# Kernel optimization log

Measured on AMD Instinct MI355X. Metric: run time of the kernel, lower is better.

## Reference

```python
import jax, jax.numpy as jnp
import numpy as np

B, N, DOP, DM, H = 8, 2048, 256, 256, 256  # batch, n_ops==n_machines, dims


def setup_inputs() -> dict:
    key = jax.random.key(0)
    ks = jax.random.split(key, 21)
    s = 0.02
    inp = {
        "operation_features": jax.random.normal(ks[0], (B, N, DOP), jnp.float32),
        "machine_features": jax.random.normal(ks[1], (B, N, DM), jnp.float32),
        "type_match_mask": jax.random.bernoulli(ks[2], 0.3, (B, N, N)).astype(jnp.float32),
        "same_type_mask": jax.random.bernoulli(ks[3], 0.3, (B, N, N)).astype(jnp.float32),
        "oma_q_w": jax.random.normal(ks[4], (H, DM), jnp.float32) * s,
        "oma_q_b": jnp.zeros((H,), jnp.float32),
        "oma_kv_w": jax.random.normal(ks[5], (2 * H, DOP), jnp.float32) * s,
        "oma_kv_b": jnp.zeros((2 * H,), jnp.float32),
        "oma_s_w": jax.random.normal(ks[6], (1, 2 * H), jnp.float32) * s,
        "oma_s_b": jnp.zeros((1,), jnp.float32),
        "oma_o_w": jax.random.normal(ks[7], (DM, H), jnp.float32) * s,
        "oma_o_b": jnp.zeros((DM,), jnp.float32),
        "sa_w_w": jax.random.normal(ks[8], (3 * H, DM), jnp.float32) * s,
        "sa_w_b": jnp.zeros((3 * H,), jnp.float32),
        "sa_s_w": jax.random.normal(ks[9], (1, 2 * H), jnp.float32) * s,
        "sa_s_b": jnp.zeros((1,), jnp.float32),
        "sa_o_w": jax.random.normal(ks[10], (DM, H), jnp.float32) * s,
        "sa_o_b": jnp.zeros((DM,), jnp.float32),
        "mix_w": jax.random.normal(ks[11], (DM, 2 * DM), jnp.float32) * s,
        "mix_b": jnp.zeros((DM,), jnp.float32),
    }
    return inp


def reference(operation_features, machine_features, type_match_mask, same_type_mask,
              oma_q_w, oma_q_b, oma_kv_w, oma_kv_b, oma_s_w, oma_s_b, oma_o_w, oma_o_b,
              sa_w_w, sa_w_b, sa_s_w, sa_s_b, sa_o_w, sa_o_b, mix_w, mix_b):
    # --- OperationMachineAttention ---
    q = machine_features @ oma_q_w.T + oma_q_b            # (B,M,H)
    kv = operation_features @ oma_kv_w.T + oma_kv_b       # (B,C,2H)
    k, v = jnp.split(kv, 2, axis=-1)
    # Linear(cat([q,k])) == q @ W[:, :H].T + k @ W[:, H:].T + b (additive-score factorization)
    sq = jnp.einsum('bmh,h->bm', q, oma_s_w[0, :H])
    sk = jnp.einsum('bch,h->bc', k, oma_s_w[0, H:])
    scores = jax.nn.leaky_relu(sq[:, :, None] + sk[:, None, :] + oma_s_b[0])  # (B,M,C)
    p = jax.nn.softmax(scores * type_match_mask, axis=-1)
    wf = jnp.einsum('bmc,bch->bmh', p, v)
    operation_machine = wf @ oma_o_w.T + oma_o_b           # (B,M,DM)

    # --- SelfAttention over machines ---
    w3 = machine_features @ sa_w_w.T + sa_w_b              # (B,C,3H)
    q2, k2, v2 = jnp.split(w3, 3, axis=-1)
    sq2 = jnp.einsum('bih,h->bi', q2, sa_s_w[0, :H])
    sk2 = jnp.einsum('bjh,h->bj', k2, sa_s_w[0, H:])
    s2 = jax.nn.leaky_relu(sq2[:, :, None] + sk2[:, None, :] + sa_s_b[0])  # (B,C,C)
    p2 = jax.nn.softmax(s2 * same_type_mask, axis=-1)
    machine_machine = jnp.einsum('bij,bjh->bih', p2, v2) @ sa_o_w.T + sa_o_b  # (B,C,DM)

    # --- mix ---
    mixed = jnp.concatenate([operation_machine, machine_machine], axis=-1)
    return mixed @ mix_w.T + mix_b                          # (B,N,DM)
```

## Files before the change

### kernel.cpp

```cpp
#include <hip/hip_runtime.h>
#include <stdint.h>
#include <stddef.h>

#define B_ 8
#define N_ 2048
#define C_ 2048
#define D_ 256
#define H_ 256

typedef __bf16 bf16x8 __attribute__((ext_vector_type(8)));
typedef __bf16 bf16x4 __attribute__((ext_vector_type(4)));
typedef float f32x4 __attribute__((ext_vector_type(4)));

#define MFMA16(a, b, c) __builtin_amdgcn_mfma_f32_16x16x32_bf16((a), (b), (c), 0, 0, 0)

__global__ __launch_bounds__(256) void k0a_partial(
    const float* __restrict__ oma_q_w, const float* __restrict__ oma_kv_w,
    const float* __restrict__ sa_w_w,
    const float* __restrict__ oma_s_w, const float* __restrict__ sa_s_w,
    float* __restrict__ partial)
{
    int d = threadIdx.x;
    int vec = blockIdx.x >> 3, hc = blockIdx.x & 7;
    int h0 = hc * 32;
    const float* Wb; const float* sv;
    if (vec == 0)      { Wb = oma_q_w  + h0 * 256;         sv = oma_s_w + h0; }
    else if (vec == 1) { Wb = oma_kv_w + h0 * 256;         sv = oma_s_w + 256 + h0; }
    else if (vec == 2) { Wb = sa_w_w   + h0 * 256;         sv = sa_s_w + h0; }
    else               { Wb = sa_w_w   + (256 + h0) * 256; sv = sa_s_w + 256 + h0; }
    float a = 0.f;
    #pragma unroll 8
    for (int h = 0; h < 32; ++h) a += Wb[h * 256 + d] * sv[h];
    partial[blockIdx.x * 256 + d] = a;
}

__global__ __launch_bounds__(256) void k0b_reduce(
    const float* __restrict__ partial,
    const float* __restrict__ oma_q_b, const float* __restrict__ oma_kv_b,
    const float* __restrict__ oma_s_w, const float* __restrict__ oma_s_b,
    const float* __restrict__ sa_w_b, const float* __restrict__ sa_s_w,
    const float* __restrict__ sa_s_b,
    float* __restrict__ wq_v, float* __restrict__ wk_v,
    float* __restrict__ wq2_v, float* __restrict__ wk2_v,
    float* __restrict__ sb)
{
    int d = threadIdx.x;
    float a0 = 0.f, a1 = 0.f, a2 = 0.f, a3 = 0.f;
    #pragma unroll
    for (int hc = 0; hc < 8; ++hc) {
        a0 += partial[(0 * 8 + hc) * 256 + d];
        a1 += partial[(1 * 8 + hc) * 256 + d];
        a2 += partial[(2 * 8 + hc) * 256 + d];
        a3 += partial[(3 * 8 + hc) * 256 + d];
    }
    wq_v[d] = a0; wk_v[d] = a1; wq2_v[d] = a2; wk2_v[d] = a3;

    int h = d;
    float p1 = oma_q_b[h] * oma_s_w[h] + oma_kv_b[h] * oma_s_w[256 + h];
    float p2 = sa_w_b[h] * sa_s_w[h] + sa_w_b[256 + h] * sa_s_w[256 + h];
    for (int o = 32; o; o >>= 1) { p1 += __shfl_xor(p1, o); p2 += __shfl_xor(p2, o); }
    __shared__ float redA[4], redB[4];
    int wv = threadIdx.x >> 6;
    if ((threadIdx.x & 63) == 0) { redA[wv] = p1; redB[wv] = p2; }
    __syncthreads();
    if (threadIdx.x == 0) {
        sb[0] = redA[0] + redA[1] + redA[2] + redA[3] + oma_s_b[0];
        sb[1] = redB[0] + redB[1] + redB[2] + redB[3] + sa_s_b[0];
    }
}

__global__ __launch_bounds__(256) void k1_wcat(
    const float* __restrict__ mix_w, const float* __restrict__ mix_b,
    const float* __restrict__ oma_o_w, const float* __restrict__ oma_o_b,
    const float* __restrict__ sa_o_w, const float* __restrict__ sa_o_b,
    __bf16* __restrict__ Wcat, float* __restrict__ b_total)
{
    int d = blockIdx.x, h = threadIdx.x;
    const float* mwr = mix_w + d * 512;
    float w1 = 0.f, w2 = 0.f;
    for (int e = 0; e < 256; ++e) {
        w1 += mwr[e] * oma_o_w[e * 256 + h];
        w2 += mwr[256 + e] * sa_o_w[e * 256 + h];
    }
    Wcat[d * 512 + h] = (__bf16)w1;
    Wcat[d * 512 + 256 + h] = (__bf16)w2;

    float pb = mwr[h] * oma_o_b[h] + mwr[256 + h] * sa_o_b[h];
    for (int o = 32; o; o >>= 1) pb += __shfl_xor(pb, o);
    __shared__ float red[4];
    if ((h & 63) == 0) red[h >> 6] = pb;
    __syncthreads();
    if (h == 0) b_total[d] = mix_b[d] + red[0] + red[1] + red[2] + red[3];
}

__global__ __launch_bounds__(256) void k2_scores(
    const float* __restrict__ op, const float* __restrict__ mach,
    const float* __restrict__ wq_v, const float* __restrict__ wk_v,
    const float* __restrict__ wq2_v, const float* __restrict__ wk2_v,
    const float* __restrict__ sb,
    float* __restrict__ sqp, float* __restrict__ skv,
    float* __restrict__ sq2p, float* __restrict__ sk2v,
    __bf16* __restrict__ opb, __bf16* __restrict__ machb)
{
    int t = threadIdx.x, lane = t & 63, wv = t >> 6;
    size_t n = (size_t)blockIdx.x * 4 + wv;
    const float4 mf = *(const float4*)(mach + n * 256 + lane * 4);
    const float4 of = *(const float4*)(op + n * 256 + lane * 4);
    const float4 q4 = *(const float4*)(wq_v + lane * 4);
    const float4 k4 = *(const float4*)(wk_v + lane * 4);
    const float4 q24 = *(const float4*)(wq2_v + lane * 4);
    const float4 k24 = *(const float4*)(wk2_v + lane * 4);

    bf16x4 mb4, ob4;
    mb4[0] = (__bf16)mf.x; mb4[1] = (__bf16)mf.y; mb4[2] = (__bf16)mf.z; mb4[3] = (__bf16)mf.w;
    ob4[0] = (__bf16)of.x; ob4[1] = (__bf16)of.y; ob4[2] = (__bf16)of.z; ob4[3] = (__bf16)of.w;
    *(bf16x4*)(machb + n * 256 + lane * 4) = mb4;
    *(bf16x4*)(opb + n * 256 + lane * 4) = ob4;

    float s1 = mf.x * q4.x + mf.y * q4.y + mf.z * q4.z + mf.w * q4.w;
    float s2 = of.x * k4.x + of.y * k4.y + of.z * k4.z + of.w * k4.w;
    float s3 = mf.x * q24.x + mf.y * q24.y + mf.z * q24.z + mf.w * q24.w;
    float s4 = mf.x * k24.x + mf.y * k24.y + mf.z * k24.z + mf.w * k24.w;
    for (int o = 32; o; o >>= 1) {
        s1 += __shfl_xor(s1, o); s2 += __shfl_xor(s2, o);
        s3 += __shfl_xor(s3, o); s4 += __shfl_xor(s4, o);
    }
    if (lane == 0) {
        sqp[n] = s1 + sb[0]; skv[n] = s2;
        sq2p[n] = s3 + sb[1]; sk2v[n] = s4;
    }
}

__global__ __launch_bounds__(256, 2) void k3_vgemm(
    const __bf16* __restrict__ opb, const __bf16* __restrict__ machb,
    const float* __restrict__ oma_kv_w, const float* __restrict__ sa_w_w,
    __bf16* __restrict__ vt)
{
    __shared__ __attribute__((aligned(16))) __bf16 As[64][72];
    __shared__ __attribute__((aligned(16))) __bf16 Bs[64][72];
    int t = threadIdx.x;
    int bid = blockIdx.x;
    int which = bid >> 10;
    int r = bid & 1023;
    int b = r >> 7;
    int ht = (r >> 5) & 3;
    int ct = r & 31;

    const float* Aglob = (which ? (sa_w_w + 512 * 256) : (oma_kv_w + 256 * 256)) + ht * 64 * 256;
    const __bf16* Bglob = (which ? machb : opb) + ((size_t)b * N_ + ct * 64) * 256;

    int lane = t & 63, wv = t >> 6;
    int l15 = lane & 15, qo = (lane >> 4) * 8;
    int rr = t >> 4;
    int dd = (t & 15) * 4;

    f32x4 acc[4] = {};

    for (int d0 = 0; d0 < 256; d0 += 64) {
        #pragma unroll
        for (int p = 0; p < 4; ++p) {
            float4 av = *(const float4*)(Aglob + (size_t)(p * 16 + rr) * 256 + d0 + dd);
            bf16x4 a4;
            a4[0] = (__bf16)av.x; a4[1] = (__bf16)av.y; a4[2] = (__bf16)av.z; a4[3] = (__bf16)av.w;
            *(bf16x4*)&As[p * 16 + rr][dd] = a4;
            bf16x4 b4 = *(const bf16x4*)(Bglob + (size_t)(p * 16 + rr) * 256 + d0 + dd);
            *(bf16x4*)&Bs[p * 16 + rr][dd] = b4;
        }
        __syncthreads();
        #pragma unroll
        for (int kb = 0; kb < 2; ++kb) {
            bf16x8 bfr = *(const bf16x8*)&Bs[16 * wv + l15][kb * 32 + qo];
            #pragma unroll
            for (int rt = 0; rt < 4; ++rt) {
                bf16x8 afr = *(const bf16x8*)&As[16 * rt + l15][kb * 32 + qo];
                acc[rt] = MFMA16(afr, bfr, acc[rt]);
            }
        }
        __syncthreads();
    }
    #pragma unroll
    for (int rt = 0; rt < 4; ++rt)
        #pragma unroll
        for (int j = 0; j < 4; ++j)
            As[16 * rt + (lane >> 4) * 4 + j][16 * wv + l15] = (__bf16)acc[rt][j];
    __syncthreads();
    int hh = t >> 2, cb = (t & 3) * 16;
    __bf16* orow = vt + (((size_t)(which * 8 + b)) * 256 + ht * 64 + hh) * 2048 + ct * 64 + cb;
    *(bf16x8*)(orow) = *(const bf16x8*)&As[hh][cb];
    *(bf16x8*)(orow + 8) = *(const bf16x8*)&As[hh][cb + 8];
}

__global__ __launch_bounds__(256, 2) void k4_attn(
    const float* __restrict__ tmask, const float* __restrict__ smask,
    const float* __restrict__ sqp, const float* __restrict__ skv,
    const float* __restrict__ sq2p, const float* __restrict__ sk2v,
    const __bf16* __restrict__ vt,
    __bf16* __restrict__ wfcat)
{
    __shared__ __attribute__((aligned(16))) __bf16 eA[64][72];
    __shared__ __attribute__((aligned(16))) __bf16 vB[256][72];
    __shared__ float rowsum[64];

    int t = threadIdx.x;
    int bid = blockIdx.x;
    int which = bid >> 8;
    int r = bid & 255;
    int b = r >> 5;
    int m0 = (r & 31) * 64;

    const float* mask = (which ? smask : tmask) + ((size_t)b * N_ + m0) * C_;
    const float* sqrow = (which ? sq2p : sqp) + b * N_ + m0;
    const float* skrow = (which ? sk2v : skv) + b * N_;
    const __bf16* vbase = vt + ((size_t)(which * 8 + b)) * 256 * 2048;

    int lane = t & 63, wv = t >> 6;
    int l15 = lane & 15, qo = (lane >> 4) * 8;
    int mrow = t >> 2;
    int cqb = (t & 3) * 16;
    int vh = t >> 3;
    int vc = (t & 7) * 8;

    float sqv = sqrow[mrow];
    float psum = 0.f;
    f32x4 acc[4][4] = {};

    bf16x8 vv[8];
    float mk[16], skc[16];

    auto load_tiles = [&](int c0) {
        #pragma unroll
        for (int p = 0; p < 8; ++p)
            vv[p] = *(const bf16x8*)(vbase + (size_t)(p * 32 + vh) * 2048 + c0 + vc);
        #pragma unroll
        for (int i = 0; i < 4; ++i) {
            float4 m4 = *(const float4*)(mask + (size_t)mrow * C_ + c0 + cqb + i * 4);
            float4 s4 = *(const float4*)(skrow + c0 + cqb + i * 4);
            mk[4 * i + 0] = m4.x; mk[4 * i + 1] = m4.y; mk[4 * i + 2] = m4.z; mk[4 * i + 3] = m4.w;
            skc[4 * i + 0] = s4.x; skc[4 * i + 1] = s4.y; skc[4 * i + 2] = s4.z; skc[4 * i + 3] = s4.w;
        }
    };
    load_tiles(0);

    for (int c0 = 0; c0 < C_; c0 += 64) {
        #pragma unroll
        for (int p = 0; p < 8; ++p)
            *(bf16x8*)&vB[p * 32 + vh][vc] = vv[p];
        bf16x8 e0, e1;
        #pragma unroll
        for (int i = 0; i < 16; ++i) {
            float s = sqv + skc[i];
            s = s > 0.f ? s : 0.01f * s;
            float e = __expf(s * mk[i]);
            psum += e;
            if (i < 8) e0[i] = (__bf16)e; else e1[i - 8] = (__bf16)e;
        }
        *(bf16x8*)&eA[mrow][cqb] = e0;
        *(bf16x8*)&eA[mrow][cqb + 8] = e1;
        __syncthreads();
        int cn = c0 + 64; if (cn >= C_) cn = 0;
        load_tiles(cn);
        #pragma unroll
        for (int kb = 0; kb < 2; ++kb) {
            bf16x8 afr[4];
            #pragma unroll
            for (int rt = 0; rt < 4; ++rt)
                afr[rt] = *(const bf16x8*)&eA[16 * rt + l15][kb * 32 + qo];
            #pragma unroll
            for (int ctile = 0; ctile < 4; ++ctile) {
                bf16x8 bfr = *(const bf16x8*)&vB[64 * wv + 16 * ctile + l15][kb * 32 + qo];
                #pragma unroll
                for (int rt = 0; rt < 4; ++rt)
                    acc[rt][ctile] = MFMA16(afr[rt], bfr, acc[rt][ctile]);
            }
        }
        __syncthreads();
    }

    float rs = psum;
    rs += __shfl_xor(rs, 1);
    rs += __shfl_xor(rs, 2);
    if ((t & 3) == 0) rowsum[mrow] = rs;
    __syncthreads();

    __bf16* obuf = &vB[0][0];
    #pragma unroll
    for (int rt = 0; rt < 4; ++rt) {
        #pragma unroll
        for (int j = 0; j < 4; ++j) {
            int m = 16 * rt + (lane >> 4) * 4 + j;
            float inv = __builtin_amdgcn_rcpf(rowsum[m]);
            #pragma unroll
            for (int ctile = 0; ctile < 4; ++ctile)
                obuf[m * 264 + 64 * wv + 16 * ctile + l15] = (__bf16)(acc[rt][ctile][j] * inv);
        }
    }
    __syncthreads();
    int m = t >> 2, cb = (t & 3) * 64;
    __bf16* wrow = wfcat + ((size_t)(b * N_ + m0 + m)) * 512 + which * 256 + cb;
    #pragma unroll
    for (int k = 0; k < 8; ++k)
        *(bf16x8*)(wrow + k * 8) = *(const bf16x8*)&obuf[m * 264 + cb + k * 8];
}

__global__ __launch_bounds__(256, 2) void k5_out(
    const __bf16* __restrict__ wfcat, const __bf16* __restrict__ Wcat,
    const float* __restrict__ b_total, float* __restrict__ out)
{
    __shared__ __attribute__((aligned(16))) __bf16 As[32][72];
    __shared__ __attribute__((aligned(16))) __bf16 Bs[256][72];
    __shared__ float bias[256];
    int t = threadIdx.x;
    int n0 = blockIdx.x * 32;
    int lane = t & 63, wv = t >> 6, l15 = lane & 15, qo = (lane >> 4) * 8;
    bias[t] = b_total[t];
    int ar = t >> 3;
    int ac = (t & 7) * 8;
    f32x4 acc[2][4] = {};

    for (int k0 = 0; k0 < 512; k0 += 64) {
        *(bf16x8*)&As[ar][ac] =
            *(const bf16x8*)(wfcat + (size_t)(n0 + ar) * 512 + k0 + ac);
        #pragma unroll
        for (int p = 0; p < 8; ++p)
            *(bf16x8*)&Bs[p * 32 + ar][ac] =
                *(const bf16x8*)(Wcat + (size_t)(p * 32 + ar) * 512 + k0 + ac);
        __syncthreads();
        #pragma unroll
        for (int kb = 0; kb < 2; ++kb) {
            bf16x8 afr[2];
            #pragma unroll
            for (int rt = 0; rt < 2; ++rt)
                afr[rt] = *(const bf16x8*)&As[16 * rt + l15][kb * 32 + qo];
            #pragma unroll
            for (int ct = 0; ct < 4; ++ct) {
                bf16x8 bfr = *(const bf16x8*)&Bs[64 * wv + 16 * ct + l15][kb * 32 + qo];
                #pragma unroll
                for (int rt = 0; rt < 2; ++rt)
                    acc[rt][ct] = MFMA16(afr[rt], bfr, acc[rt][ct]);
            }
        }
        __syncthreads();
    }
    #pragma unroll
    for (int rt = 0; rt < 2; ++rt) {
        #pragma unroll
        for (int ct = 0; ct < 4; ++ct) {
            int d = 64 * wv + 16 * ct + l15;
            float bv = bias[d];
            #pragma unroll
            for (int j = 0; j < 4; ++j) {
                int m = 16 * rt + (lane >> 4) * 4 + j;
                out[(size_t)(n0 + m) * 256 + d] = acc[rt][ct][j] + bv;
            }
        }
    }
}

extern "C" void kernel_launch(void* const* d_in, const int* in_sizes, int n_in,
                              void* d_out, int out_size, void* d_ws, size_t ws_size,
                              hipStream_t stream)
{
    const float* op_feat  = (const float*)d_in[0];
    const float* mach_feat= (const float*)d_in[1];
    const float* tmask    = (const float*)d_in[2];
    const float* smask    = (const float*)d_in[3];
    const float* oma_q_w  = (const float*)d_in[4];
    const float* oma_q_b  = (const float*)d_in[5];
    const float* oma_kv_w = (const float*)d_in[6];
    const float* oma_kv_b = (const float*)d_in[7];
    const float* oma_s_w  = (const float*)d_in[8];
    const float* oma_s_b  = (const float*)d_in[9];
    const float* oma_o_w  = (const float*)d_in[10];
    const float* oma_o_b  = (const float*)d_in[11];
    const float* sa_w_w   = (const float*)d_in[12];
    const float* sa_w_b   = (const float*)d_in[13];
    const float* sa_s_w   = (const float*)d_in[14];
    const float* sa_s_b   = (const float*)d_in[15];
    const float* sa_o_w   = (const float*)d_in[16];
    const float* sa_o_b   = (const float*)d_in[17];
    const float* mix_w    = (const float*)d_in[18];
    const float* mix_b    = (const float*)d_in[19];

    char* ws = (char*)d_ws;
    float* wq_v   = (float*)(ws + 0);
    float* wk_v   = (float*)(ws + 1024);
    float* wq2_v  = (float*)(ws + 2048);
    float* wk2_v  = (float*)(ws + 3072);
    float* sb     = (float*)(ws + 4096);
    float* btot   = (float*)(ws + 4352);
    float* sqp    = (float*)(ws + 8192);
    float* skv    = (float*)(ws + 73728);
    float* sq2p   = (float*)(ws + 139264);
    float* sk2v   = (float*)(ws + 204800);
    __bf16* Wcat  = (__bf16*)(ws + 270336);
    __bf16* vt    = (__bf16*)(ws + 532480);
    __bf16* wfcat = (__bf16*)(ws + 17309696);
    float* outp   = (float*)d_out;

    float* partial = (float*)(ws + 532480);
    __bf16* opb   = (__bf16*)(ws + 17309696);
    __bf16* machb = (__bf16*)(ws + 17309696 + 8388608);

    k0a_partial<<<32, 256, 0, stream>>>(oma_q_w, oma_kv_w, sa_w_w,
                                        oma_s_w, sa_s_w, partial);
    k0b_reduce<<<1, 256, 0, stream>>>(partial, oma_q_b, oma_kv_b, oma_s_w, oma_s_b,
                                      sa_w_b, sa_s_w, sa_s_b,
                                      wq_v, wk_v, wq2_v, wk2_v, sb);
    k1_wcat<<<256, 256, 0, stream>>>(mix_w, mix_b, oma_o_w, oma_o_b,
                                     sa_o_w, sa_o_b, Wcat, btot);
    k2_scores<<<4096, 256, 0, stream>>>(op_feat, mach_feat, wq_v, wk_v, wq2_v, wk2_v,
                                        sb, sqp, skv, sq2p, sk2v, opb, machb);
    k3_vgemm<<<2048, 256, 0, stream>>>(opb, machb, oma_kv_w, sa_w_w, vt);
    k4_attn<<<512, 256, 0, stream>>>(tmask, smask, sqp, skv, sq2p, sk2v, vt, wfcat);
    k5_out<<<512, 256, 0, stream>>>(wfcat, Wcat, btot, outp);
}
```

Before: 413.5 us.

## Double-buffer mask/score loads two tiles ahead and use LDS-only barriers

Splits the per-tile load into V loads and mask/sk loads, keeping two register buffers for mask and sk so those global loads are issued two tiles ahead. The loop is unrolled by two to alternate between the buffers. __syncthreads is replaced with an lgkmcnt(0) wait plus s_barrier, so barriers no longer wait on outstanding global loads (vmcnt). The aim is to hide global memory latency behind the MFMA work, at the cost of more registers and reliance on the compiler to insert the correct vmcnt waits before the loaded values are used.

```diff
diff --git a/kernel.cpp b/kernel.cpp
--- a/kernel.cpp
+++ b/kernel.cpp
@@ -225,12 +225,14 @@
     f32x4 acc[4][4] = {};
 
     bf16x8 vv[8];
-    float mk[16], skc[16];
-
-    auto load_tiles = [&](int c0) {
+    float mkA[16], skA[16], mkB[16], skB[16];
+
+    auto load_v = [&](int c0) {
         #pragma unroll
         for (int p = 0; p < 8; ++p)
             vv[p] = *(const bf16x8*)(vbase + (size_t)(p * 32 + vh) * 2048 + c0 + vc);
+    };
+    auto load_ms = [&](float* mk, float* skc, int c0) {
         #pragma unroll
         for (int i = 0; i < 4; ++i) {
             float4 m4 = *(const float4*)(mask + (size_t)mrow * C_ + c0 + cqb + i * 4);
@@ -239,12 +241,12 @@
             skc[4 * i + 0] = s4.x; skc[4 * i + 1] = s4.y; skc[4 * i + 2] = s4.z; skc[4 * i + 3] = s4.w;
         }
     };
-    load_tiles(0);
-
-    for (int c0 = 0; c0 < C_; c0 += 64) {
+    auto stage_v = [&]() {
         #pragma unroll
         for (int p = 0; p < 8; ++p)
             *(bf16x8*)&vB[p * 32 + vh][vc] = vv[p];
+    };
+    auto compute_e = [&](const float* mk, const float* skc) {
         bf16x8 e0, e1;
         #pragma unroll
         for (int i = 0; i < 16; ++i) {
@@ -256,9 +258,8 @@
         }
         *(bf16x8*)&eA[mrow][cqb] = e0;
         *(bf16x8*)&eA[mrow][cqb + 8] = e1;
-        __syncthreads();
-        int cn = c0 + 64; if (cn >= C_) cn = 0;
-        load_tiles(cn);
+    };
+    auto do_mfma = [&]() {
         #pragma unroll
         for (int kb = 0; kb < 2; ++kb) {
             bf16x8 afr[4];
@@ -273,7 +274,32 @@
                     acc[rt][ctile] = MFMA16(afr[rt], bfr, acc[rt][ctile]);
             }
         }
-        __syncthreads();
+    };
+    auto lgkm_barrier = []() {
+        asm volatile("s_waitcnt lgkmcnt(0)" ::: "memory");
+        __builtin_amdgcn_s_barrier();
+    };
+
+    load_v(0);
+    load_ms(mkA, skA, 0);
+    load_ms(mkB, skB, 64);
+
+    #pragma unroll 1
+    for (int c0 = 0; c0 < C_; c0 += 128) {
+        stage_v();
+        compute_e(mkA, skA);
+        lgkm_barrier();
+        load_v((c0 + 64) & (C_ - 1));
+        load_ms(mkA, skA, (c0 + 128) & (C_ - 1));
+        do_mfma();
+        lgkm_barrier();
+        stage_v();
+        compute_e(mkB, skB);
+        lgkm_barrier();
+        load_v((c0 + 128) & (C_ - 1));
+        load_ms(mkB, skB, (c0 + 192) & (C_ - 1));
+        do_mfma();
+        lgkm_barrier();
     }
 
     float rs = psum;
```

Measured after the change: 427.5 us. 1.03x slower.
